# Optimization experiments

Measured on AMD Instinct MI355X. Metric: run time of the kernel, lower is better.

The kernel has to match this reference:

```python
import jax, jax.numpy as jnp
import numpy as np

LAT = 4; K = 4; NP = 3 * K - 1; HID = 16; NT = 10; BOUND = 5.0
_in_deg = np.arange(1, LAT + 1)
_hd = (np.arange(HID) % (LAT - 1)) + 1
M1 = jnp.asarray((_hd[:, None] >= _in_deg[None, :]).astype(np.float32))  # [HID, LAT]
M2 = jnp.asarray((_hd[:, None] >= _hd[None, :]).astype(np.float32))      # [HID, HID]
M3 = jnp.asarray((np.repeat(_in_deg, NP)[:, None] > _hd[None, :]).astype(np.float32))  # [LAT*NP, HID]


def _subm(x, m, w, b):
    # submanifold conv: inactive inputs are zero, output restricted to active sites
    y = jax.lax.conv_general_dilated(x, w, (1, 1), 'SAME', dimension_numbers=('NHWC', 'HWIO', 'NHWC')) + b
    return jnp.where(m[..., None], y, 0.0)


def _maxpool(x, m, kh, kw):
    neg = jnp.asarray(-1e30, x.dtype)
    xm = jnp.where(m[..., None], x, neg)
    y = jax.lax.reduce_window(xm, neg, jax.lax.max, (1, kh, kw, 1), (1, kh, kw, 1), 'VALID')
    mo = jax.lax.reduce_window(m.astype(x.dtype), 0.0, jax.lax.max, (1, kh, kw), (1, kh, kw), 'VALID') > 0
    return jnp.where(mo[..., None], y, 0.0), mo


def _invconv(x, w, b, mo):
    # sparse inverse conv with kernel == stride of paired pool: non-overlapping transposed conv
    kh, kw, ci, co = w.shape
    B, h, wd, _ = x.shape
    y = jnp.einsum('bhwc,ijcd->bhiwjd', x, w).reshape(B, h * kh, wd * kw, co) + b
    return jnp.where(mo[..., None], y, 0.0)


def _rqs(x, uw, uh, ud):
    # monotonic rational-quadratic spline, identity outside [-BOUND, BOUND]
    shp = x.shape
    widths = jax.nn.softmax(uw, -1) * (2 * BOUND)
    heights = jax.nn.softmax(uh, -1) * (2 * BOUND)
    edge = jnp.full(shp + (1,), -BOUND, x.dtype)
    xk = jnp.concatenate([edge, jnp.cumsum(widths, -1) - BOUND], -1)
    yk = jnp.concatenate([edge, jnp.cumsum(heights, -1) - BOUND], -1)
    one = jnp.ones(shp + (1,), x.dtype)
    dk = jnp.concatenate([one, jax.nn.softplus(ud), one], -1)
    inside = (x >= -BOUND) & (x <= BOUND)
    xc = jnp.clip(x, -BOUND, BOUND)
    idx = jnp.clip(jnp.sum((xc[..., None] >= xk[..., :-1]).astype(jnp.int32), -1) - 1, 0, K - 1)[..., None]
    g = lambda a, i: jnp.take_along_axis(a, i, -1)[..., 0]
    x0, x1 = g(xk, idx), g(xk, idx + 1)
    y0, y1 = g(yk, idx), g(yk, idx + 1)
    d0, d1 = g(dk, idx), g(dk, idx + 1)
    dx = x1 - x0
    dy = y1 - y0
    s = dy / dx
    t = (xc - x0) / dx
    den = s + (d1 + d0 - 2 * s) * t * (1 - t)
    y = y0 + dy * (s * t * t + d0 * t * (1 - t)) / den
    ld = jnp.log(s * s * (d1 * t * t + 2 * s * t * (1 - t) + d0 * (1 - t) ** 2)) - 2 * jnp.log(den)
    return jnp.where(inside, y, x), jnp.where(inside, ld, 0.0)


def _nsf(z, fW1, fb1, fW2, fb2, fW3, fb3):
    ld_tot = jnp.zeros(z.shape[:-1], z.dtype)
    for t in range(NT):
        h = jax.nn.relu(z @ (fW1[t] * M1).T + fb1[t])
        h = jax.nn.relu(h @ (fW2[t] * M2).T + fb2[t])
        p = (h @ (fW3[t] * M3).T + fb3[t]).reshape(z.shape[:-1] + (LAT, NP))
        z, ld = _rqs(z, p[..., :K], p[..., K:2 * K], p[..., 2 * K:])
        ld_tot = ld_tot + ld.sum(-1)
        if t < NT - 1:
            z = z[..., ::-1]
    return z, ld_tot


def _forward(x, eps, w1, b1, w2, b2, w3, b3, wmu, bmu, wlv, blv, wlin, blin, u1, bu1, w4, b4, u2, bu2, w5, b5, u3, bu3, w6, b6, fW1, fb1, fW2, fb2, fW3, fb3):
    xn = jnp.transpose(x, (0, 2, 3, 1))  # NCHW -> NHWC
    m0 = jnp.any(xn != 0, axis=-1)       # active sites (spconv from_dense)
    lrelu = lambda v: jax.nn.leaky_relu(v, 0.01)
    y = lrelu(_subm(xn, m0, w1, b1))
    y, m1 = _maxpool(y, m0, 2, 2)
    y = lrelu(_subm(y, m1, w2, b2))
    y, m2 = _maxpool(y, m1, 5, 2)
    y = lrelu(_subm(y, m2, w3, b3))
    y, m3 = _maxpool(y, m2, 5, 2)        # [B, 4, 16, 32]
    mu = jnp.where(m3[..., None], y @ wmu.T + bmu, 0.0)
    logvar = jnp.where(m3[..., None], y @ wlv.T + blv, 0.0)
    std = jnp.exp(0.5 * logvar)
    z0 = mu + eps * std
    z, log_det = _nsf(z0, fW1, fb1, fW2, fb2, fW3, fb3)
    LOG2PI = 1.8378770664093453
    log_q0 = jnp.sum(-0.5 * ((z0 - mu) / std) ** 2 - jnp.log(std) - 0.5 * LOG2PI, -1)
    log_p = jnp.sum(-0.5 * z * z - 0.5 * LOG2PI, -1)
    kld_pc = log_q0 - log_det - log_p
    kld = jnp.sum(jnp.where(m3, kld_pc, 0.0), axis=(1, 2))  # index_add over batch indices
    zf = jnp.where(m3[..., None], z, 0.0)
    dec = jnp.where(m3[..., None], zf @ wlin.T + blin, 0.0)
    y = _invconv(dec, u1, bu1, m2)
    y = _subm(y, m2, w4, b4)
    y = _invconv(y, u2, bu2, m1)
    y = _subm(y, m1, w5, b5)
    y = _invconv(y, u3, bu3, m0)
    y = _subm(y, m0, w6, b6)
    out = jnp.transpose(y, (0, 3, 1, 2))  # back to NCHW like .dense()
    return out, mu, logvar, kld, zf


def setup_inputs():
    key = jax.random.key(0)
    ks = iter(jax.random.split(key, 80))
    B, C, H, W = 128, 6, 200, 128
    d = {}
    x = jax.random.normal(next(ks), (B, C, H, W), jnp.float32)
    keep = jax.random.uniform(next(ks), (B, 1, H, W)) < 0.15
    d['x'] = jnp.where(keep, x, 0.0)
    d['eps'] = jax.random.normal(next(ks), (B, 4, 16, LAT), jnp.float32)
    def p(name, shape, s=0.1):
        d[name] = jax.random.normal(next(ks), shape, jnp.float32) * s
    p('w1', (3, 3, 6, 8)); p('b1', (8,))
    p('w2', (3, 3, 8, 16)); p('b2', (16,))
    p('w3', (3, 3, 16, 32)); p('b3', (32,))
    p('wmu', (LAT, 32)); p('bmu', (LAT,))
    p('wlv', (LAT, 32)); p('blv', (LAT,))
    p('wlin', (32, LAT)); p('blin', (32,))
    p('u1', (5, 2, 32, 32)); p('bu1', (32,))
    p('w4', (3, 3, 32, 16)); p('b4', (16,))
    p('u2', (5, 2, 16, 16)); p('bu2', (16,))
    p('w5', (3, 3, 16, 8)); p('b5', (8,))
    p('u3', (2, 2, 8, 8)); p('bu3', (8,))
    p('w6', (3, 3, 8, 6)); p('b6', (6,))
    p('fW1', (NT, HID, LAT)); p('fb1', (NT, HID))
    p('fW2', (NT, HID, HID)); p('fb2', (NT, HID))
    p('fW3', (NT, LAT * NP, HID)); p('fb3', (NT, LAT * NP))
    return d


def reference(x, eps, w1, b1, w2, b2, w3, b3, wmu, bmu, wlv, blv, wlin, blin, u1, bu1, w4, b4, u2, bu2, w5, b5, u3, bu3, w6, b6, fW1, fb1, fW2, fb2, fW3, fb3):
    return _forward(x, eps, w1, b1, w2, b2, w3, b3, wmu, bmu, wlv, blv, wlin, blin, u1, bu1, w4, b4, u2, bu2, w5, b5, u3, bu3, w6, b6, fW1, fb1, fW2, fb2, fW3, fb3)
```

## Files before the change

kernel.cpp:

```cpp
#include <hip/hip_runtime.h>
#include <math.h>

constexpr int NB=128;
constexpr int NH0=200, NW0=128, NC0=6;
constexpr int NH1=100, NW1=64,  NC1=8;
constexpr int NH2=20,  NW2=32,  NC2=16;
constexpr int NH3=4,   NW3=16,  NC3=32;
constexpr int LAT=4, NPp=11, HID=16, NT=10;
constexpr float BOUNDf=5.0f;
constexpr float LOG2PI=1.8378770664093453f;

__device__ __forceinline__ float fexpf(float v){ return __expf(v); }
__device__ __forceinline__ float flogf(float v){ return __logf(v); }
__device__ __forceinline__ float softplusf(float v){ return v>20.f ? v : __logf(1.f+__expf(v)); }
__device__ __forceinline__ float lrelu(float v){ return v>0.f ? v : 0.01f*v; }

__global__ __launch_bounds__(256) void k_conv1pool(
    const float* __restrict__ x, const float* __restrict__ w1, const float* __restrict__ b1,
    float* __restrict__ y1p, unsigned char* __restrict__ m0, unsigned char* __restrict__ m1){
  __shared__ float xs[6][34][34];
  __shared__ float ws1[54][8];
  __shared__ unsigned char ms[34][34];
  int blk = blockIdx.x;
  int b  = blk / 28;
  int t  = blk % 28;
  int th = t / 4, tw = t % 4;
  int hp0 = th*16, wp0 = tw*16;
  int h0 = hp0*2 - 1, w0 = wp0*2 - 1;
  int tid = threadIdx.x;
  for (int i=tid;i<432;i+=256) ws1[i>>3][i&7] = w1[i];
  for (int i=tid;i<6*34*34;i+=256){
    int ci=i/1156; int rem=i-ci*1156; int r=rem/34, c=rem-r*34;
    int h=h0+r, w=w0+c;
    float v=0.f;
    if (h>=0 && h<NH0 && w>=0 && w<NW0) v = x[((size_t)(b*NC0+ci)*NH0+h)*NW0+w];
    xs[ci][r][c]=v;
  }
  __syncthreads();
  for (int i=tid;i<1156;i+=256){
    int r=i/34, c=i-r*34;
    bool any=false;
    #pragma unroll
    for (int ci=0;ci<6;ci++) any |= (xs[ci][r][c]!=0.f);
    ms[r][c] = any?1:0;
  }
  __syncthreads();
  for (int i=tid;i<1024;i+=256){
    int r=(i>>5)+1, c=(i&31)+1;
    int h=h0+r, w=w0+c;
    if (h<NH0) m0[(b*NH0+h)*NW0+w] = ms[r][c];
  }
  int lhp = tid>>4, lwp = tid&15;
  int hp = hp0+lhp, wp = wp0+lwp;
  if (hp < NH1){
    float best[8];
    #pragma unroll
    for (int co=0;co<8;co++) best[co]=-1e30f;
    bool many=false;
    #pragma unroll 1
    for (int i=0;i<2;i++)
    #pragma unroll 1
    for (int j=0;j<2;j++){
      int r = lhp*2+i+1, c = lwp*2+j+1;
      if (!ms[r][c]) continue;
      many=true;
      float a[8];
      #pragma unroll
      for (int co=0;co<8;co++) a[co]=b1[co];
      #pragma unroll 1
      for (int kh=0;kh<3;kh++)
      #pragma unroll 1
      for (int kw=0;kw<3;kw++){
        #pragma unroll
        for (int ci=0;ci<6;ci++){
          float v = xs[ci][r-1+kh][c-1+kw];
          const float* wv = ws1[(kh*3+kw)*6+ci];
          #pragma unroll
          for (int co=0;co<8;co++) a[co]=fmaf(v,wv[co],a[co]);
        }
      }
      #pragma unroll
      for (int co=0;co<8;co++) best[co]=fmaxf(best[co], lrelu(a[co]));
    }
    float* yp = y1p + (((size_t)b*NH1+hp)*NW1+wp)*8;
    #pragma unroll
    for (int co=0;co<8;co++) yp[co] = many?best[co]:0.f;
    m1[(b*NH1+hp)*NW1+wp] = many?1:0;
  }
}

__global__ __launch_bounds__(256) void k_conv2pool(
    const float* __restrict__ yin, const unsigned char* __restrict__ m1,
    const float* __restrict__ w2, const float* __restrict__ b2,
    float* __restrict__ yout, unsigned char* __restrict__ m2){
  __shared__ float ys[8][27][35];
  __shared__ unsigned char msl[27][35];
  __shared__ float w2s[72][16];
  __shared__ float b2s[16];
  int blk = blockIdx.x;
  int b  = blk >> 3;
  int t  = blk & 7;
  int th = t >> 1, tw = t & 1;
  int r0 = th*25 - 1, c0 = tw*32 - 1;
  int tid = threadIdx.x;
  for (int i=tid;i<1152;i+=256) w2s[i>>4][i&15] = w2[i];
  if (tid<16) b2s[tid]=b2[tid];
  for (int p=tid;p<27*34;p+=256){
    int r=p/34, c=p-(p/34)*34;
    int h1=r0+r, w1c=c0+c;
    bool ok = (h1>=0 && h1<NH1 && w1c>=0 && w1c<NW1);
    msl[r][c] = ok ? m1[(b*NH1+h1)*NW1+w1c] : 0;
    float4 v0=make_float4(0,0,0,0), v1=v0;
    if (ok){
      const float4* pp = (const float4*)(yin + (((size_t)b*NH1+h1)*NW1+w1c)*8);
      v0=pp[0]; v1=pp[1];
    }
    ys[0][r][c]=v0.x; ys[1][r][c]=v0.y; ys[2][r][c]=v0.z; ys[3][r][c]=v0.w;
    ys[4][r][c]=v1.x; ys[5][r][c]=v1.y; ys[6][r][c]=v1.z; ys[7][r][c]=v1.w;
  }
  __syncthreads();
  if (tid < 160){
    int oid = tid >> 1, coq = tid & 1;
    int co0 = coq*8;
    int lh = oid >> 4, lw = oid & 15;
    int h2 = th*5+lh, w2c = tw*16+lw;
    float best[8];
    #pragma unroll
    for (int co=0;co<8;co++) best[co]=-1e30f;
    bool many=false;
    #pragma unroll 1
    for (int i=0;i<5;i++)
    #pragma unroll 1
    for (int j=0;j<2;j++){
      int r = lh*5+i+1, c = lw*2+j+1;
      if (!msl[r][c]) continue;
      many=true;
      float a[8];
      #pragma unroll
      for (int co=0;co<8;co++) a[co]=b2s[co0+co];
      #pragma unroll 1
      for (int kh=0;kh<3;kh++)
      #pragma unroll 1
      for (int kw=0;kw<3;kw++){
        #pragma unroll
        for (int ci=0;ci<8;ci++){
          float v = ys[ci][r-1+kh][c-1+kw];
          const float* wr = w2s[(kh*3+kw)*8+ci];
          #pragma unroll
          for (int co=0;co<8;co++) a[co]=fmaf(v,wr[co0+co],a[co]);
        }
      }
      #pragma unroll
      for (int co=0;co<8;co++) best[co]=fmaxf(best[co], lrelu(a[co]));
    }
    float4 o0,o1;
    if (many){
      o0=make_float4(best[0],best[1],best[2],best[3]);
      o1=make_float4(best[4],best[5],best[6],best[7]);
    } else { o0=make_float4(0,0,0,0); o1=o0; }
    float4* op = (float4*)(yout + (((size_t)b*NH2+h2)*NW2+w2c)*16 + co0);
    op[0]=o0; op[1]=o1;
    if (coq==0) m2[(b*NH2+h2)*NW2+w2c] = many?1:0;
  }
}

__global__ __launch_bounds__(256) void k_conv3pool(
    const float* __restrict__ yin, const unsigned char* __restrict__ m2,
    const float* __restrict__ w3, const float* __restrict__ b3,
    float* __restrict__ yout, unsigned char* __restrict__ m3,
    float* __restrict__ out_kld){
  __shared__ float ys[16][20][33];
  __shared__ unsigned char msl[20][32];
  __shared__ float w3s[144][32];
  __shared__ float b3s[32];
  int b = blockIdx.x;
  int tid = threadIdx.x;
  if (tid==0) out_kld[b]=0.f;
  for (int i=tid;i<4608;i+=256) w3s[i>>5][i&31] = w3[i];
  if (tid<32) b3s[tid]=b3[tid];
  for (int p=tid;p<640;p+=256){
    int r=p>>5, c=p&31;
    msl[r][c] = m2[(b*NH2+r)*NW2+c];
    const float4* pp = (const float4*)(yin + (((size_t)b*NH2+r)*NW2+c)*16);
    float4 q0=pp[0],q1=pp[1],q2=pp[2],q3=pp[3];
    ys[0][r][c]=q0.x; ys[1][r][c]=q0.y; ys[2][r][c]=q0.z; ys[3][r][c]=q0.w;
    ys[4][r][c]=q1.x; ys[5][r][c]=q1.y; ys[6][r][c]=q1.z; ys[7][r][c]=q1.w;
    ys[8][r][c]=q2.x; ys[9][r][c]=q2.y; ys[10][r][c]=q2.z; ys[11][r][c]=q2.w;
    ys[12][r][c]=q3.x; ys[13][r][c]=q3.y; ys[14][r][c]=q3.z; ys[15][r][c]=q3.w;
  }
  __syncthreads();
  int p = tid>>2, coq = tid&3;
  int co0 = coq*8;
  int hp = p>>4, wp = p&15;
  float best[8];
  #pragma unroll
  for (int co=0;co<8;co++) best[co]=-1e30f;
  bool many=false;
  #pragma unroll 1
  for (int i=0;i<5;i++)
  #pragma unroll 1
  for (int j=0;j<2;j++){
    int h2 = hp*5+i, w2c = wp*2+j;
    if (!msl[h2][w2c]) continue;
    many=true;
    float a[8];
    #pragma unroll
    for (int co=0;co<8;co++) a[co]=b3s[co0+co];
    #pragma unroll 1
    for (int kh=0;kh<3;kh++){
      int hh=h2+kh-1;
      if (hh<0||hh>=NH2) continue;
      #pragma unroll 1
      for (int kw=0;kw<3;kw++){
        int ww=w2c+kw-1;
        if (ww<0||ww>=NW2) continue;
        #pragma unroll
        for (int ci=0;ci<16;ci++){
          float v = ys[ci][hh][ww];
          const float* wr = w3s[(kh*3+kw)*16+ci];
          #pragma unroll
          for (int co=0;co<8;co++) a[co]=fmaf(v,wr[co0+co],a[co]);
        }
      }
    }
    #pragma unroll
    for (int co=0;co<8;co++) best[co]=fmaxf(best[co], lrelu(a[co]));
  }
  float4 o0,o1;
  if (many){
    o0=make_float4(best[0],best[1],best[2],best[3]);
    o1=make_float4(best[4],best[5],best[6],best[7]);
  } else { o0=make_float4(0,0,0,0); o1=o0; }
  float4* op = (float4*)(yout + ((size_t)(b*64+p))*32 + co0);
  op[0]=o0; op[1]=o1;
  if (coq==0) m3[b*64+p] = many?1:0;
}

__global__ __launch_bounds__(64) void k_latent(
    const float* __restrict__ y3p, const unsigned char* __restrict__ m3,
    const float* __restrict__ eps,
    const float* __restrict__ wmu, const float* __restrict__ bmu,
    const float* __restrict__ wlv, const float* __restrict__ blv,
    const float* __restrict__ wlin, const float* __restrict__ blin,
    const float* __restrict__ fW1, const float* __restrict__ fb1,
    const float* __restrict__ fW2, const float* __restrict__ fb2,
    const float* __restrict__ fW3, const float* __restrict__ fb3,
    float* __restrict__ out_mu, float* __restrict__ out_lv,
    float* __restrict__ out_kld, float* __restrict__ out_zf,
    float* __restrict__ dec)
{
  __shared__ __align__(16) float sW1[NT*HID*LAT];
  __shared__ float sb1[NT*HID];
  __shared__ __align__(16) float sW2[NT*HID*HID];
  __shared__ float sb2[NT*HID];
  __shared__ __align__(16) float sW3[NT*LAT*NPp*HID];
  __shared__ float sb3[NT*LAT*NPp];
  __shared__ __align__(16) float swmu[LAT*NC3];
  __shared__ __align__(16) float swlv[LAT*NC3];
  __shared__ __align__(16) float slin[NC3*LAT];
  __shared__ float sbmu[LAT], sblv[LAT], sblin[NC3];
  int tid = threadIdx.x;
  for (int i=tid;i<NT*HID*LAT;i+=64){ int j=i&3; int r=(i>>2)%HID; sW1[i]=fW1[i]*(((r%3+1)>=(j+1))?1.f:0.f); }
  for (int i=tid;i<NT*HID;i+=64){ sb1[i]=fb1[i]; sb2[i]=fb2[i]; }
  for (int i=tid;i<NT*HID*HID;i+=64){ int j=i&15; int r=(i>>4)%HID; sW2[i]=fW2[i]*(((r%3+1)>=(j%3+1))?1.f:0.f); }
  for (int i=tid;i<NT*LAT*NPp*HID;i+=64){ int j=i&15; int r=(i>>4)%(LAT*NPp); sW3[i]=fW3[i]*(((r/NPp+1)>(j%3+1))?1.f:0.f); }
  for (int i=tid;i<NT*LAT*NPp;i+=64) sb3[i]=fb3[i];
  for (int i=tid;i<LAT*NC3;i+=64){ swmu[i]=wmu[i]; swlv[i]=wlv[i]; slin[i]=wlin[i]; }
  if (tid<LAT){ sbmu[tid]=bmu[tid]; sblv[tid]=blv[tid]; }
  for (int i=tid;i<NC3;i+=64) sblin[i]=blin[i];
  __syncthreads();

  int blk = blockIdx.x;
  int b   = blk >> 2;
  int gpos = b*64 + (blk&3)*16 + (tid>>2);
  int g = tid & 3;
  bool msk = m3[gpos]!=0;
  float kld_part = 0.f;
  if (msk){
    const float4* yp = (const float4*)(y3p + (size_t)gpos*NC3);
    const float4* wm = (const float4*)(swmu + g*NC3);
    const float4* wl = (const float4*)(swlv + g*NC3);
    float mu_g = sbmu[g], lv_g = sblv[g];
    #pragma unroll
    for (int q=0;q<8;q++){
      float4 yq = yp[q], a = wm[q], c = wl[q];
      mu_g = fmaf(yq.x,a.x, fmaf(yq.y,a.y, fmaf(yq.z,a.z, fmaf(yq.w,a.w, mu_g))));
      lv_g = fmaf(yq.x,c.x, fmaf(yq.y,c.y, fmaf(yq.z,c.z, fmaf(yq.w,c.w, lv_g))));
    }
    float std_g = fexpf(0.5f*lv_g);
    float ev_g  = eps[(size_t)gpos*LAT+g];
    float z0_g  = fmaf(ev_g, std_g, mu_g);
    float zg = z0_g;
    float z[4];
    z[g]=zg; z[g^1]=__shfl_xor(zg,1); z[g^2]=__shfl_xor(zg,2); z[g^3]=__shfl_xor(zg,3);
    float ld_g = 0.f;
    for (int t=0;t<NT;t++){
      float h1[16];
      const float4* W1t = (const float4*)(sW1 + t*HID*LAT);
      const float*  b1t = sb1 + t*HID;
      #pragma unroll
      for (int i2=0;i2<16;i2++){
        float4 w = W1t[i2];
        float a = b1t[i2];
        a = fmaf(z[0],w.x, fmaf(z[1],w.y, fmaf(z[2],w.z, fmaf(z[3],w.w, a))));
        h1[i2]=fmaxf(a,0.f);
      }
      float h2o[4];
      const float* W2t = sW2 + t*HID*HID;
      const float* b2t = sb2 + t*HID;
      #pragma unroll
      for (int k=0;k<4;k++){
        int row = g*4+k;
        const float4* wr = (const float4*)(W2t + row*HID);
        float a = b2t[row];
        #pragma unroll
        for (int q=0;q<4;q++){
          float4 w = wr[q];
          a = fmaf(h1[q*4+0],w.x, fmaf(h1[q*4+1],w.y, fmaf(h1[q*4+2],w.z, fmaf(h1[q*4+3],w.w, a))));
        }
        h2o[k]=fmaxf(a,0.f);
      }
      float h2[16];
      #pragma unroll
      for (int k=0;k<4;k++) h2[g*4+k]=h2o[k];
      #pragma unroll
      for (int mski=1;mski<4;mski++){
        int og = g^mski;
        #pragma unroll
        for (int k=0;k<4;k++) h2[og*4+k]=__shfl_xor(h2o[k],mski);
      }
      float p[NPp];
      const float* W3t = sW3 + t*LAT*NPp*HID;
      const float* b3t = sb3 + t*LAT*NPp;
      #pragma unroll
      for (int r=0;r<NPp;r++){
        int row = g*NPp+r;
        const float4* wr = (const float4*)(W3t + row*HID);
        float a = b3t[row];
        #pragma unroll
        for (int q=0;q<4;q++){
          float4 w = wr[q];
          a = fmaf(h2[q*4+0],w.x, fmaf(h2[q*4+1],w.y, fmaf(h2[q*4+2],w.z, fmaf(h2[q*4+3],w.w, a))));
        }
        p[r]=a;
      }
      float mw=fmaxf(fmaxf(p[0],p[1]),fmaxf(p[2],p[3]));
      float e0=fexpf(p[0]-mw), e1=fexpf(p[1]-mw), e2=fexpf(p[2]-mw), e3=fexpf(p[3]-mw);
      float wsc=10.f/(e0+e1+e2+e3);
      float xk1=fmaf(e0,wsc,-BOUNDf), xk2=fmaf(e1,wsc,xk1), xk3=fmaf(e2,wsc,xk2), xk4=fmaf(e3,wsc,xk3);
      float mh=fmaxf(fmaxf(p[4],p[5]),fmaxf(p[6],p[7]));
      float f0=fexpf(p[4]-mh), f1=fexpf(p[5]-mh), f2=fexpf(p[6]-mh), f3=fexpf(p[7]-mh);
      float hsc=10.f/(f0+f1+f2+f3);
      float yk1=fmaf(f0,hsc,-BOUNDf), yk2=fmaf(f1,hsc,yk1), yk3=fmaf(f2,hsc,yk2), yk4=fmaf(f3,hsc,yk3);
      float dk1=softplusf(p[8]), dk2=softplusf(p[9]), dk3=softplusf(p[10]);
      float xv=z[g];
      bool inside = (xv>=-BOUNDf)&&(xv<=BOUNDf);
      float xc=fminf(fmaxf(xv,-BOUNDf),BOUNDf);
      float x0=-BOUNDf, x1=xk1, y0=-BOUNDf, y1=yk1, d0=1.f, d1=dk1;
      if (xc>=xk1){x0=xk1;x1=xk2;y0=yk1;y1=yk2;d0=dk1;d1=dk2;}
      if (xc>=xk2){x0=xk2;x1=xk3;y0=yk2;y1=yk3;d0=dk2;d1=dk3;}
      if (xc>=xk3){x0=xk3;x1=xk4;y0=yk3;y1=yk4;d0=dk3;d1=1.f;}
      float dxv=x1-x0, dyv=y1-y0;
      float sl=dyv/dxv, ttv=(xc-x0)/dxv, omt=1.f-ttv;
      float den=sl + (d1+d0-2.f*sl)*ttv*omt;
      float yo=y0 + dyv*(sl*ttv*ttv + d0*ttv*omt)/den;
      float ldv=flogf(sl*sl*(d1*ttv*ttv + 2.f*sl*ttv*omt + d0*omt*omt)) - 2.f*flogf(den);
      float zn_g = inside ? yo : xv;
      ld_g += inside ? ldv : 0.f;
      float znf[4];
      znf[g]=zn_g; znf[g^1]=__shfl_xor(zn_g,1); znf[g^2]=__shfl_xor(zn_g,2); znf[g^3]=__shfl_xor(zn_g,3);
      if (t<NT-1){ z[0]=znf[3]; z[1]=znf[2]; z[2]=znf[1]; z[3]=znf[0]; }
      else       { z[0]=znf[0]; z[1]=znf[1]; z[2]=znf[2]; z[3]=znf[3]; }
    }
    float lq_g = -0.5f*ev_g*ev_g - 0.5f*lv_g - 0.5f*LOG2PI;
    float lp_g = -0.5f*z[g]*z[g] - 0.5f*LOG2PI;
    kld_part = lq_g - ld_g - lp_g;
    out_mu[(size_t)gpos*LAT+g]=mu_g;
    out_lv[(size_t)gpos*LAT+g]=lv_g;
    out_zf[(size_t)gpos*LAT+g]=z[g];
    float4 d0v, d1v;
    {
      float dv[8];
      #pragma unroll
      for (int k=0;k<8;k++){
        int c = g*8+k;
        const float4 w = ((const float4*)slin)[c];
        dv[k] = fmaf(z[0],w.x, fmaf(z[1],w.y, fmaf(z[2],w.z, fmaf(z[3],w.w, sblin[c]))));
      }
      d0v=make_float4(dv[0],dv[1],dv[2],dv[3]);
      d1v=make_float4(dv[4],dv[5],dv[6],dv[7]);
    }
    float4* dp = (float4*)(dec + (size_t)gpos*NC3 + g*8);
    dp[0]=d0v; dp[1]=d1v;
  } else {
    out_mu[(size_t)gpos*LAT+g]=0.f;
    out_lv[(size_t)gpos*LAT+g]=0.f;
    out_zf[(size_t)gpos*LAT+g]=0.f;
    float4 zv = make_float4(0,0,0,0);
    float4* dp = (float4*)(dec + (size_t)gpos*NC3 + g*8);
    dp[0]=zv; dp[1]=zv;
  }
  float s = kld_part;
  s += __shfl_xor(s,1);  s += __shfl_xor(s,2);
  s += __shfl_xor(s,4);  s += __shfl_xor(s,8);
  s += __shfl_xor(s,16); s += __shfl_xor(s,32);
  if (tid==0) atomicAdd(&out_kld[b], s);
}

__global__ __launch_bounds__(256) void k_ic4(
    const float* __restrict__ dec, const unsigned char* __restrict__ m2,
    const float* __restrict__ u1, const float* __restrict__ bu1,
    const float* __restrict__ w4, const float* __restrict__ b4,
    float* __restrict__ t2){
  __shared__ __align__(16) float vs[12][18][32];
  __shared__ __align__(16) float w4s[288][16];
  __shared__ unsigned char msl[12][18];
  int blk = blockIdx.x;
  int b  = blk >> 2;
  int t  = blk & 3;
  int th = t >> 1, tw = t & 1;
  int h0 = th*10, w0 = tw*16;
  int tid = threadIdx.x;
  for (int i=tid;i<288*16;i+=256) w4s[i>>4][i&15] = w4[i];
  if (tid < 216){
    int lr = tid/18, lc = tid%18;
    int h2 = h0-1+lr, w2 = w0-1+lc;
    bool mk = (h2>=0 && h2<NH2 && w2>=0 && w2<NW2) && m2[(b*NH2+h2)*NW2+w2];
    msl[lr][lc] = mk?1:0;
    float acc[32];
    if (mk){
      const float* dp = dec + (((size_t)b*NH3 + h2/5)*NW3 + w2/2)*NC3;
      const float* up = u1 + ((h2%5)*2 + (w2&1))*1024;
      #pragma unroll
      for (int co=0;co<32;co++) acc[co]=bu1[co];
      #pragma unroll 1
      for (int ci=0;ci<32;ci++){
        float dv = dp[ci];
        const float* ur = up + ci*32;
        #pragma unroll
        for (int co=0;co<32;co++) acc[co]=fmaf(dv,ur[co],acc[co]);
      }
    } else {
      #pragma unroll
      for (int co=0;co<32;co++) acc[co]=0.f;
    }
    #pragma unroll
    for (int co=0;co<32;co++) vs[lr][lc][co]=acc[co];
  }
  __syncthreads();
  if (tid < 160){
    int lh = tid/16, lw = tid%16;
    int h2 = h0+lh, w2 = w0+lw;
    float a[16];
    if (msl[lh+1][lw+1]){
      #pragma unroll
      for (int co=0;co<16;co++) a[co]=b4[co];
      #pragma unroll 1
      for (int kh=0;kh<3;kh++)
      #pragma unroll 1
      for (int kw=0;kw<3;kw++){
        const float* vp = vs[lh+kh][lw+kw];
        #pragma unroll
        for (int ci=0;ci<32;ci++){
          float v = vp[ci];
          const float* wr = w4s[(kh*3+kw)*32+ci];
          #pragma unroll
          for (int co=0;co<16;co++) a[co]=fmaf(v,wr[co],a[co]);
        }
      }
    } else {
      #pragma unroll
      for (int co=0;co<16;co++) a[co]=0.f;
    }
    float* op = t2 + (((size_t)b*NH2+h2)*NW2+w2)*NC2;
    #pragma unroll
    for (int co=0;co<16;co++) op[co]=a[co];
  }
}

__global__ __launch_bounds__(256) void k_ic5(
    const float* __restrict__ t2, const unsigned char* __restrict__ m1,
    const float* __restrict__ u2, const float* __restrict__ bu2,
    const float* __restrict__ w5, const float* __restrict__ b5,
    float* __restrict__ t4){
  __shared__ __align__(16) float vs[12][18][16];
  __shared__ __align__(16) float w5s[144][8];
  __shared__ unsigned char msl[12][18];
  int blk = blockIdx.x;
  int b  = blk / 40;
  int t  = blk % 40;
  int th = t >> 2, tw = t & 3;
  int h0 = th*10, w0 = tw*16;
  int tid = threadIdx.x;
  for (int i=tid;i<144*8;i+=256) w5s[i>>3][i&7] = w5[i];
  if (tid < 216){
    int lr = tid/18, lc = tid%18;
    int h1 = h0-1+lr, w1c = w0-1+lc;
    bool mk = (h1>=0 && h1<NH1 && w1c>=0 && w1c<NW1) && m1[(b*NH1+h1)*NW1+w1c];
    msl[lr][lc] = mk?1:0;
    float acc[16];
    if (mk){
      const float* dp = t2 + (((size_t)b*NH2 + h1/5)*NW2 + w1c/2)*NC2;
      const float* up = u2 + ((h1%5)*2 + (w1c&1))*256;
      #pragma unroll
      for (int co=0;co<16;co++) acc[co]=bu2[co];
      #pragma unroll 1
      for (int ci=0;ci<16;ci++){
        float dv = dp[ci];
        const float* ur = up + ci*16;
        #pragma unroll
        for (int co=0;co<16;co++) acc[co]=fmaf(dv,ur[co],acc[co]);
      }
    } else {
      #pragma unroll
      for (int co=0;co<16;co++) acc[co]=0.f;
    }
    #pragma unroll
    for (int co=0;co<16;co++) vs[lr][lc][co]=acc[co];
  }
  __syncthreads();
  if (tid < 160){
    int lh = tid/16, lw = tid%16;
    int h1 = h0+lh, w1c = w0+lw;
    float a[8];
    if (msl[lh+1][lw+1]){
      #pragma unroll
      for (int co=0;co<8;co++) a[co]=b5[co];
      #pragma unroll 1
      for (int kh=0;kh<3;kh++)
      #pragma unroll 1
      for (int kw=0;kw<3;kw++){
        const float* vp = vs[lh+kh][lw+kw];
        #pragma unroll
        for (int ci=0;ci<16;ci++){
          float v = vp[ci];
          const float* wr = w5s[(kh*3+kw)*16+ci];
          #pragma unroll
          for (int co=0;co<8;co++) a[co]=fmaf(v,wr[co],a[co]);
        }
      }
    } else {
      #pragma unroll
      for (int co=0;co<8;co++) a[co]=0.f;
    }
    float* op = t4 + (((size_t)b*NH1+h1)*NW1+w1c)*NC1;
    #pragma unroll
    for (int co=0;co<8;co++) op[co]=a[co];
  }
}

__global__ __launch_bounds__(256) void k_inv3conv6(
    const float* __restrict__ t4, const unsigned char* __restrict__ m0,
    const float* __restrict__ u3, const float* __restrict__ bu3,
    const float* __restrict__ w6, const float* __restrict__ b6,
    float* __restrict__ out){
  __shared__ float vs[8][18][68];
  __shared__ unsigned char msl[18][66];
  __shared__ float u3s[4][8][8];
  __shared__ float w6s[9][8][6];
  __shared__ float bu3s[8];
  __shared__ float b6s[6];
  int blk = blockIdx.x;
  int b  = blk / 26;
  int t  = blk % 26;
  int th = t >> 1, tw = t & 1;
  int h0 = th*16, w0 = tw*64;
  int tid = threadIdx.x;
  for (int i=tid;i<256;i+=256){ u3s[i>>6][(i>>3)&7][i&7]=u3[i]; }
  for (int i=tid;i<432;i+=256){ int tap=i/48; int rem=i%48; w6s[tap][rem/6][rem%6]=w6[i]; }
  if (tid<8) bu3s[tid]=bu3[tid];
  if (tid<6) b6s[tid]=b6[tid];
  __syncthreads();
  for (int p=tid;p<18*66;p+=256){
    int r=p/66, c=p-(p/66)*66;
    int h=h0-1+r, w=w0-1+c;
    bool act = (h>=0 && h<NH0 && w>=0 && w<NW0) && m0[(b*NH0+h)*NW0+w];
    msl[r][c] = act?1:0;
    float v8[8];
    if (act){
      const float4* tp = (const float4*)(t4 + (((size_t)b*NH1 + (h>>1))*NW1 + (w>>1))*8);
      float4 q0=tp[0], q1=tp[1];
      float tin[8]={q0.x,q0.y,q0.z,q0.w,q1.x,q1.y,q1.z,q1.w};
      const float (*up)[8] = u3s[(h&1)*2+(w&1)];
      #pragma unroll
      for (int c8=0;c8<8;c8++) v8[c8]=bu3s[c8];
      #pragma unroll
      for (int ci=0;ci<8;ci++){
        float v=tin[ci];
        #pragma unroll
        for (int c8=0;c8<8;c8++) v8[c8]=fmaf(v, up[ci][c8], v8[c8]);
      }
    } else {
      #pragma unroll
      for (int c8=0;c8<8;c8++) v8[c8]=0.f;
    }
    #pragma unroll
    for (int c8=0;c8<8;c8++) vs[c8][r][c]=v8[c8];
  }
  __syncthreads();
  #pragma unroll 1
  for (int k=0;k<4;k++){
    int p = tid + k*256;
    int lh = p>>6, lw = p&63;
    int h = h0+lh, w = w0+lw;
    if (h >= NH0) continue;
    float acc[6];
    if (msl[lh+1][lw+1]){
      #pragma unroll
      for (int co=0;co<6;co++) acc[co]=b6s[co];
      #pragma unroll 1
      for (int kh=0;kh<3;kh++)
      #pragma unroll 1
      for (int kw=0;kw<3;kw++){
        const float (*wt)[6] = w6s[kh*3+kw];
        #pragma unroll
        for (int ci=0;ci<8;ci++){
          float v = vs[ci][lh+kh][lw+kw];
          #pragma unroll
          for (int co=0;co<6;co++) acc[co]=fmaf(v, wt[ci][co], acc[co]);
        }
      }
    } else {
      #pragma unroll
      for (int co=0;co<6;co++) acc[co]=0.f;
    }
    size_t base = (size_t)b*6*NH0*NW0 + (size_t)h*NW0 + w;
    #pragma unroll
    for (int co=0;co<6;co++) out[base + (size_t)co*NH0*NW0] = acc[co];
  }
}

extern "C" void kernel_launch(void* const* d_in, const int* in_sizes, int n_in,
                              void* d_out, int out_size, void* d_ws, size_t ws_size,
                              hipStream_t stream){
  (void)in_sizes; (void)n_in; (void)out_size; (void)ws_size;
  const float* x    = (const float*)d_in[0];
  const float* eps  = (const float*)d_in[1];
  const float* w1   = (const float*)d_in[2];
  const float* b1   = (const float*)d_in[3];
  const float* w2   = (const float*)d_in[4];
  const float* b2   = (const float*)d_in[5];
  const float* w3   = (const float*)d_in[6];
  const float* b3   = (const float*)d_in[7];
  const float* wmu  = (const float*)d_in[8];
  const float* bmu  = (const float*)d_in[9];
  const float* wlv  = (const float*)d_in[10];
  const float* blv  = (const float*)d_in[11];
  const float* wlin = (const float*)d_in[12];
  const float* blin = (const float*)d_in[13];
  const float* u1   = (const float*)d_in[14];
  const float* bu1  = (const float*)d_in[15];
  const float* w4   = (const float*)d_in[16];
  const float* b4   = (const float*)d_in[17];
  const float* u2   = (const float*)d_in[18];
  const float* bu2  = (const float*)d_in[19];
  const float* w5   = (const float*)d_in[20];
  const float* b5   = (const float*)d_in[21];
  const float* u3   = (const float*)d_in[22];
  const float* bu3  = (const float*)d_in[23];
  const float* w6   = (const float*)d_in[24];
  const float* b6   = (const float*)d_in[25];
  const float* fW1  = (const float*)d_in[26];
  const float* fb1  = (const float*)d_in[27];
  const float* fW2  = (const float*)d_in[28];
  const float* fb2  = (const float*)d_in[29];
  const float* fW3  = (const float*)d_in[30];
  const float* fb3  = (const float*)d_in[31];

  char* ws = (char*)d_ws;
  unsigned char* m0 = (unsigned char*)(ws);
  unsigned char* m1 = (unsigned char*)(ws + 3276800);
  unsigned char* m2 = (unsigned char*)(ws + 4096000);
  unsigned char* m3 = (unsigned char*)(ws + 4177920);
  float* y1p = (float*)(ws + 4194304);
  float* y2p = (float*)(ws + 30408704);
  float* y3p = (float*)(ws + 35651584);
  float* dec = (float*)(ws + 36700160);
  float* t2  = y2p;
  float* t4  = y1p;

  float* out   = (float*)d_out;
  float* o_mu  = out + 19660800;
  float* o_lv  = out + 19693568;
  float* o_kld = out + 19726336;
  float* o_zf  = out + 19726464;

  k_conv1pool<<< 3584,256,0,stream>>>(x, w1, b1, y1p, m0, m1);
  k_conv2pool<<< 1024,256,0,stream>>>(y1p, m1, w2, b2, y2p, m2);
  k_conv3pool<<<  128,256,0,stream>>>(y2p, m2, w3, b3, y3p, m3, o_kld);
  k_latent   <<<  512, 64,0,stream>>>(y3p, m3, eps, wmu,bmu,wlv,blv,wlin,blin,
                                      fW1,fb1,fW2,fb2,fW3,fb3, o_mu,o_lv,o_kld,o_zf, dec);
  k_ic4      <<<  512,256,0,stream>>>(dec, m2, u1, bu1, w4, b4, t2);
  k_ic5      <<< 5120,256,0,stream>>>(t2, m1, u2, bu2, w5, b5, t4);
  k_inv3conv6<<< 3328,256,0,stream>>>(t4, m0, u3, bu3, w6, b6, out);
}
```

Measured before the change: 454.4 us.

## Map one thread per full-res pixel in conv1 and pool via wave shuffles

Measured after the change: 449.5 us. About the same (-1.1%).

```diff
diff --git a/kernel.cpp b/kernel.cpp
--- a/kernel.cpp
+++ b/kernel.cpp
@@ -18,74 +18,72 @@
 __global__ __launch_bounds__(256) void k_conv1pool(
     const float* __restrict__ x, const float* __restrict__ w1, const float* __restrict__ b1,
     float* __restrict__ y1p, unsigned char* __restrict__ m0, unsigned char* __restrict__ m1){
-  __shared__ float xs[6][34][34];
+  __shared__ float xs[6][18][24];
   __shared__ float ws1[54][8];
-  __shared__ unsigned char ms[34][34];
+  __shared__ float b1s[8];
   int blk = blockIdx.x;
-  int b  = blk / 28;
-  int t  = blk % 28;
-  int th = t / 4, tw = t % 4;
-  int hp0 = th*16, wp0 = tw*16;
-  int h0 = hp0*2 - 1, w0 = wp0*2 - 1;
+  int b  = blk / 104;
+  int t  = blk % 104;
+  int th = t >> 3, tw = t & 7;
+  int h0 = th*16, w0 = tw*16;
   int tid = threadIdx.x;
   for (int i=tid;i<432;i+=256) ws1[i>>3][i&7] = w1[i];
-  for (int i=tid;i<6*34*34;i+=256){
-    int ci=i/1156; int rem=i-ci*1156; int r=rem/34, c=rem-r*34;
-    int h=h0+r, w=w0+c;
+  if (tid<8) b1s[tid]=b1[tid];
+  for (int i=tid;i<6*18*18;i+=256){
+    int ci=i/324; int rem=i-ci*324; int r=rem/18, c=rem-r*18;
+    int h=h0-1+r, w=w0-1+c;
     float v=0.f;
     if (h>=0 && h<NH0 && w>=0 && w<NW0) v = x[((size_t)(b*NC0+ci)*NH0+h)*NW0+w];
     xs[ci][r][c]=v;
   }
   __syncthreads();
-  for (int i=tid;i<1156;i+=256){
-    int r=i/34, c=i-r*34;
-    bool any=false;
-    #pragma unroll
-    for (int ci=0;ci<6;ci++) any |= (xs[ci][r][c]!=0.f);
-    ms[r][c] = any?1:0;
-  }
-  __syncthreads();
-  for (int i=tid;i<1024;i+=256){
-    int r=(i>>5)+1, c=(i&31)+1;
-    int h=h0+r, w=w0+c;
-    if (h<NH0) m0[(b*NH0+h)*NW0+w] = ms[r][c];
-  }
-  int lhp = tid>>4, lwp = tid&15;
-  int hp = hp0+lhp, wp = wp0+lwp;
-  if (hp < NH1){
-    float best[8];
-    #pragma unroll
-    for (int co=0;co<8;co++) best[co]=-1e30f;
-    bool many=false;
-    #pragma unroll 1
-    for (int i=0;i<2;i++)
-    #pragma unroll 1
-    for (int j=0;j<2;j++){
-      int r = lhp*2+i+1, c = lwp*2+j+1;
-      if (!ms[r][c]) continue;
-      many=true;
-      float a[8];
-      #pragma unroll
-      for (int co=0;co<8;co++) a[co]=b1[co];
-      #pragma unroll 1
-      for (int kh=0;kh<3;kh++)
-      #pragma unroll 1
-      for (int kw=0;kw<3;kw++){
-        #pragma unroll
-        for (int ci=0;ci<6;ci++){
-          float v = xs[ci][r-1+kh][c-1+kw];
-          const float* wv = ws1[(kh*3+kw)*6+ci];
-          #pragma unroll
-          for (int co=0;co<8;co++) a[co]=fmaf(v,wv[co],a[co]);
-        }
-      }
-      #pragma unroll
-      for (int co=0;co<8;co++) best[co]=fmaxf(best[co], lrelu(a[co]));
-    }
-    float* yp = y1p + (((size_t)b*NH1+hp)*NW1+wp)*8;
-    #pragma unroll
-    for (int co=0;co<8;co++) yp[co] = many?best[co]:0.f;
-    m1[(b*NH1+hp)*NW1+wp] = many?1:0;
+  int r = tid>>4, c = tid&15;
+  int h = h0+r, w = w0+c;
+  bool inb = (h < NH0);
+  float c0v=xs[0][r+1][c+1], c1v=xs[1][r+1][c+1], c2v=xs[2][r+1][c+1];
+  float c3v=xs[3][r+1][c+1], c4v=xs[4][r+1][c+1], c5v=xs[5][r+1][c+1];
+  bool act = inb && ((c0v!=0.f)||(c1v!=0.f)||(c2v!=0.f)||(c3v!=0.f)||(c4v!=0.f)||(c5v!=0.f));
+  if (inb) m0[(b*NH0+h)*NW0+w] = act?1:0;
+  float a[8];
+  #pragma unroll
+  for (int co=0;co<8;co++) a[co]=b1s[co];
+  #pragma unroll 1
+  for (int kh=0;kh<3;kh++)
+  #pragma unroll 1
+  for (int kw=0;kw<3;kw++){
+    #pragma unroll
+    for (int ci=0;ci<6;ci++){
+      float v = xs[ci][r+kh][c+kw];
+      const float* wv = ws1[(kh*3+kw)*6+ci];
+      #pragma unroll
+      for (int co=0;co<8;co++) a[co]=fmaf(v,wv[co],a[co]);
+    }
+  }
+  #pragma unroll
+  for (int co=0;co<8;co++) a[co] = act ? lrelu(a[co]) : -1e30f;
+  float best[8];
+  #pragma unroll
+  for (int co=0;co<8;co++){
+    float v = a[co];
+    v = fmaxf(v, __shfl_xor(v,1));
+    v = fmaxf(v, __shfl_xor(v,16));
+    best[co]=v;
+  }
+  float af = act?1.f:0.f;
+  af = fmaxf(af, __shfl_xor(af,1));
+  af = fmaxf(af, __shfl_xor(af,16));
+  bool anyact = af>0.f;
+  bool rep = ((r&1)==0) && ((c&1)==0);
+  if (rep && inb){
+    int hp=h>>1, wp=w>>1;
+    float4 o0,o1;
+    if (anyact){
+      o0=make_float4(best[0],best[1],best[2],best[3]);
+      o1=make_float4(best[4],best[5],best[6],best[7]);
+    } else { o0=make_float4(0,0,0,0); o1=o0; }
+    float4* yp = (float4*)(y1p + (((size_t)b*NH1+hp)*NW1+wp)*8);
+    yp[0]=o0; yp[1]=o1;
+    m1[(b*NH1+hp)*NW1+wp] = anyact?1:0;
   }
 }
 
@@ -685,7 +683,7 @@
   float* o_kld = out + 19726336;
   float* o_zf  = out + 19726464;
 
-  k_conv1pool<<< 3584,256,0,stream>>>(x, w1, b1, y1p, m0, m1);
+  k_conv1pool<<<13312,256,0,stream>>>(x, w1, b1, y1p, m0, m1);
   k_conv2pool<<< 1024,256,0,stream>>>(y1p, m1, w2, b2, y2p, m2);
   k_conv3pool<<<  128,256,0,stream>>>(y2p, m2, w3, b3, y3p, m3, o_kld);
   k_latent   <<<  512, 64,0,stream>>>(y3p, m3, eps, wmu,bmu,wlv,blv,wlin,blin,
```
